# Optimization experiments

Hardware: AMD Instinct MI355X
Metric: run time of the kernel (lower is better)

Reference implementation:

```python
import jax, jax.numpy as jnp
import numpy as np

H = 128          # hidden_channels
K = 3            # TAGConv hops
NV, NS = 100000, 50000
EVV, ESS, EH, EIN = 1_000_000, 500_000, 500_000, 300_000


def setup_inputs() -> dict:
    key = jax.random.key(0)
    ks = iter(jax.random.split(key, 40))
    def rn(shape, s=0.05):
        return jax.random.normal(next(ks), shape, jnp.float32) * s
    def ri(shape, hi):
        return jax.random.randint(next(ks), shape, 0, hi, jnp.int32)
    return {
        "game_x": rn((NV, 5), 1.0),
        "state_x": rn((NS, 6), 1.0),
        "edge_index_v_v": ri((2, EVV), NV),
        "edge_type_v_v": ri((EVV,), 4),  # unused in forward (interface fidelity)
        "edge_index_history_v_s": jnp.stack([ri((EH,), NV), ri((EH,), NS)]),
        "edge_attr_history_v_s": rn((EH, 1), 1.0),
        "edge_index_in_v_s": jnp.stack([ri((EIN,), NV), ri((EIN,), NS)]),
        "edge_index_s_s": ri((2, ESS), NS),
        # TAGConv weights: (K+1) hop linears, shared bias
        "tag1_W": rn((K + 1, 5, H)), "tag1_b": rn((H,)),
        "tag2_W": rn((K + 1, 6, H)), "tag2_b": rn((H,)),
        # 7 SAGEConv layers stacked: gv[1:3]=0,1; sv[1:3]=2,3; in1=4; sv2=5,6
        "sage_Wl": rn((7, H, H)), "sage_bl": rn((7, H)), "sage_Wr": rn((7, H, H)),
        # GATConv (1 head, edge_dim=1)
        "gat_Wsrc": rn((H, H)), "gat_Wdst": rn((H, H)), "gat_We": rn((1, H)),
        "gat_asrc": rn((H,)), "gat_adst": rn((H,)), "gat_ae": rn((H,)), "gat_b": rn((H,)),
        # final MLP: single Linear(H, 1)
        "mlp_W": rn((H, 1)), "mlp_b": rn((1,)),
    }


def _seg_sum(x, idx, n):
    return jax.ops.segment_sum(x, idx, num_segments=n)


def tag_conv(x, edge_index, n, W, b):
    """TAGConv: out = sum_k lin_k(A_norm^k x) + b, gcn_norm w/o self loops."""
    src, dst = edge_index[0], edge_index[1]
    deg = _seg_sum(jnp.ones(src.shape, x.dtype), dst, n)
    dinv = jnp.where(deg > 0, jax.lax.rsqrt(jnp.maximum(deg, 1.0)), 0.0)
    norm = dinv[src] * dinv[dst]                      # [E]
    out = x @ W[0]
    h = x
    for k in range(1, W.shape[0]):
        h = _seg_sum(h[src] * norm[:, None], dst, n)  # one hop of normalized A
        out = out + h @ W[k]
    return out + b


def sage_conv(x_src, x_dst, edge_index, n_dst, Wl, bl, Wr):
    """SAGEConv(mean): lin_l(mean_j x_src[j]) + lin_r(x_dst)."""
    src, dst = edge_index[0], edge_index[1]
    s = _seg_sum(x_src[src], dst, n_dst)
    cnt = _seg_sum(jnp.ones(src.shape, x_src.dtype), dst, n_dst)
    mean = s / jnp.maximum(cnt, 1.0)[:, None]
    return mean @ Wl + bl + x_dst @ Wr


def gat_conv(x_src, x_dst, edge_index, edge_attr, n_dst,
             Wsrc, Wdst, We, asrc, adst, ae, b):
    """Bipartite GATConv, 1 head, edge features, no self loops."""
    src, dst = edge_index[0], edge_index[1]
    hs = x_src @ Wsrc                                  # [NV, H]
    hd = x_dst @ Wdst                                  # [NS, H]
    a = (hs @ asrc)[src] + (hd @ adst)[dst] + (edge_attr @ We) @ ae  # [E]
    a = jax.nn.leaky_relu(a, 0.2)
    m = jax.ops.segment_max(a, dst, num_segments=n_dst)
    e = jnp.exp(a - m[dst])                            # segment softmax
    denom = _seg_sum(e, dst, n_dst)
    alpha = e / jnp.maximum(denom, 1e-16)[dst]
    out = _seg_sum(alpha[:, None] * hs[src], dst, n_dst)
    return out + b


def reference(game_x, state_x, edge_index_v_v, edge_type_v_v,
              edge_index_history_v_s, edge_attr_history_v_s,
              edge_index_in_v_s, edge_index_s_s,
              tag1_W, tag1_b, tag2_W, tag2_b,
              sage_Wl, sage_bl, sage_Wr,
              gat_Wsrc, gat_Wdst, gat_We, gat_asrc, gat_adst, gat_ae, gat_b,
              mlp_W, mlp_b):
    relu = jax.nn.relu
    nv, ns = game_x.shape[0], state_x.shape[0]
    # game-vertex tower
    gx = relu(tag_conv(game_x, edge_index_v_v, nv, tag1_W, tag1_b))
    for i in range(2):
        gx = relu(sage_conv(gx, gx, edge_index_v_v, nv, sage_Wl[i], sage_bl[i], sage_Wr[i]))
    # state-vertex tower
    sx = relu(tag_conv(state_x, edge_index_s_s, ns, tag2_W, tag2_b))
    for i in range(2, 4):
        sx = relu(sage_conv(sx, sx, edge_index_s_s, ns, sage_Wl[i], sage_bl[i], sage_Wr[i]))
    # bipartite attention game -> state
    hist = relu(gat_conv(gx, sx, edge_index_history_v_s, edge_attr_history_v_s, ns,
                         gat_Wsrc, gat_Wdst, gat_We, gat_asrc, gat_adst, gat_ae, gat_b))
    in_x = relu(sage_conv(gx, hist, edge_index_in_v_s, ns, sage_Wl[4], sage_bl[4], sage_Wr[4]))
    # second state tower
    sx = in_x
    for i in range(5, 7):
        sx = relu(sage_conv(sx, sx, edge_index_s_s, ns, sage_Wl[i], sage_bl[i], sage_Wr[i]))
    return sx @ mlp_W + mlp_b                          # [NS, 1]
```

## Files before the change

kernel.cpp:

```cpp
#include <hip/hip_runtime.h>

#define H 128
typedef unsigned short u16;
typedef __attribute__((ext_vector_type(8))) short bf16x8;
typedef __attribute__((ext_vector_type(4))) float f32x4;


static inline int gridFor(long long work, int block, int cap = 8192){
  long long g = (work + block - 1) / block;
  if (g > cap) g = cap;
  if (g < 1) g = 1;
  return (int)g;
}

__device__ __forceinline__ float waveReduceSum(float v){
  #pragma unroll
  for(int off = 32; off > 0; off >>= 1) v += __shfl_down(v, off);
  return v;
}

__device__ __forceinline__ float bflo(unsigned v){ return __uint_as_float(v << 16); }
__device__ __forceinline__ float bfhi(unsigned v){ return __uint_as_float(v & 0xffff0000u); }
__device__ __forceinline__ u16 f2bf(float f){
  unsigned u = __float_as_uint(f);
  return (u16)((u + 0x7fffu + ((u >> 16) & 1u)) >> 16);
}
__device__ __forceinline__ unsigned pack2(float lo, float hi){
  return (unsigned)f2bf(lo) | ((unsigned)f2bf(hi) << 16);
}

#define BSHIFT 9
#define CH 2048

template<bool HAS_ATTR>
__global__ __launch_bounds__(256) void part_kernel(
    const int* __restrict__ src, const int* __restrict__ dst,
    const float* __restrict__ attr, int* __restrict__ bcur,
    int2* __restrict__ bpairs, float* __restrict__ battr, int E, int cap){
  __shared__ int hist[256];
  __shared__ int hscan[256];
  __shared__ int hbase[256];
  __shared__ int hcur[256];
  __shared__ int2 buf[CH];
  __shared__ float abuf[HAS_ATTR ? CH : 1];

  const int t = threadIdx.x;
  const int e0 = blockIdx.x * CH;
  const int cnt = min(CH, E - e0);

  hist[t] = 0; hcur[t] = 0;
  __syncthreads();

  #pragma unroll
  for(int j = 0; j < 8; j++){
    int i = e0 + j*256 + t;
    if(i - e0 < cnt) atomicAdd(&hist[dst[i] >> BSHIFT], 1);
  }
  __syncthreads();

  {
    int v = hist[t];
    int lane = t & 63, wid = t >> 6;
    int incl = v;
    #pragma unroll
    for(int off = 1; off < 64; off <<= 1){
      int u = __shfl_up(incl, off);
      if(lane >= off) incl += u;
    }
    __shared__ int ws4[4];
    if(lane == 63) ws4[wid] = incl;
    __syncthreads();
    int wofs = 0;
    for(int wj = 0; wj < wid; wj++) wofs += ws4[wj];
    hscan[t] = wofs + incl - v;
    hbase[t] = (v > 0) ? atomicAdd(&bcur[t], v) : 0;
  }
  __syncthreads();

  #pragma unroll
  for(int j = 0; j < 8; j++){
    int i = e0 + j*256 + t;
    if(i - e0 < cnt){
      int d = dst[i], s = src[i];
      int b = d >> BSHIFT;
      int lp = atomicAdd(&hcur[b], 1);
      int slot = hscan[b] + lp;
      buf[slot] = make_int2(d, s);
      if(HAS_ATTR) abuf[slot] = attr[i];
    }
  }
  __syncthreads();

  for(int u = t; u < cnt; u += 256){
    int2 pr = buf[u];
    int b = pr.x >> BSHIFT;
    int g = b * cap + hbase[b] + (u - hscan[b]);
    bpairs[g] = pr;
    if(HAS_ATTR) battr[g] = abuf[u];
  }
}

__global__ void bucket_scan(const int* __restrict__ bcur, int* __restrict__ bbase,
                            int* __restrict__ rp0, int* __restrict__ rp1,
                            int* __restrict__ rp2, int* __restrict__ rp3,
                            int n0, int n1, int n2, int n3){
  int g = blockIdx.x;
  int n = (g == 0) ? n0 : (g == 1) ? n1 : (g == 2) ? n2 : n3;
  int* rowp = (g == 0) ? rp0 : (g == 1) ? rp1 : (g == 2) ? rp2 : rp3;
  int NB = (n + 511) >> BSHIFT;
  int t = threadIdx.x;
  int v = (t < NB) ? bcur[g*256 + t] : 0;
  int lane = t & 63, wid = t >> 6;
  int incl = v;
  #pragma unroll
  for(int off = 1; off < 64; off <<= 1){
    int u = __shfl_up(incl, off);
    if(lane >= off) incl += u;
  }
  __shared__ int ws4[4];
  if(lane == 63) ws4[wid] = incl;
  __syncthreads();
  int wofs = 0;
  for(int wj = 0; wj < wid; wj++) wofs += ws4[wj];
  bbase[g*256 + t] = wofs + incl - v;
  if(t == 0) rowp[n] = ws4[0] + ws4[1] + ws4[2] + ws4[3];
}

template<bool HAS_ATTR, bool DINV>
__global__ __launch_bounds__(256) void build_kernel(
    const int2* __restrict__ bpairs, const float* __restrict__ battr,
    const int* __restrict__ bcur, const int* __restrict__ bbase,
    int* __restrict__ rowp, int* __restrict__ col, float* __restrict__ attrp,
    float* __restrict__ dinv, int cap, int n){
  __shared__ int hist[512];
  __shared__ int hcur[512];
  __shared__ int ws4[4];

  const int b = blockIdx.x;
  const int t = threadIdx.x;
  const int d0 = b << BSHIFT;
  const int dn = min(512, n - d0);
  const int cnt = bcur[b];
  const int base = bbase[b];
  const int2* ep = bpairs + (size_t)b * cap;

  hist[t] = 0; hist[t + 256] = 0;
  __syncthreads();
  for(int u = t; u < cnt; u += 256) atomicAdd(&hist[ep[u].x - d0], 1);
  __syncthreads();

  int a0 = hist[2*t], a1 = hist[2*t + 1];
  int s = a0 + a1;
  int lane = t & 63, wid = t >> 6;
  int incl = s;
  #pragma unroll
  for(int off = 1; off < 64; off <<= 1){
    int u = __shfl_up(incl, off);
    if(lane >= off) incl += u;
  }
  if(lane == 63) ws4[wid] = incl;
  __syncthreads();
  int wofs = 0;
  for(int wj = 0; wj < wid; wj++) wofs += ws4[wj];
  int excl = wofs + incl - s;
  __syncthreads();
  hcur[2*t] = excl; hcur[2*t + 1] = excl + a0;
  if(2*t < dn){
    rowp[d0 + 2*t] = base + excl;
    if(DINV) dinv[d0 + 2*t] = a0 > 0 ? rsqrtf((float)a0) : 0.f;
  }
  if(2*t + 1 < dn){
    rowp[d0 + 2*t + 1] = base + excl + a0;
    if(DINV) dinv[d0 + 2*t + 1] = a1 > 0 ? rsqrtf((float)a1) : 0.f;
  }
  __syncthreads();

  for(int u = t; u < cnt; u += 256){
    int2 pr = ep[u];
    int pos = base + atomicAdd(&hcur[pr.x - d0], 1);
    col[pos] = pr.y;
    if(HAS_ATTR) attrp[pos] = battr[(size_t)b * cap + u];
  }
}


__global__ void cvt_weights(const float* __restrict__ Wl, const float* __restrict__ Wr,
                            const float* __restrict__ Wsrc, u16* __restrict__ Wb){
  const int total = 15 * H * H;
  for(int t = blockIdx.x*blockDim.x + threadIdx.x; t < total; t += gridDim.x*blockDim.x){
    int mat = t >> 14, idx = t & 16383;
    int k = idx >> 7, colj = idx & 127;
    const float* srcp = (mat < 7) ? (Wl + ((size_t)mat << 14))
                       : (mat < 14) ? (Wr + ((size_t)(mat - 7) << 14))
                       : Wsrc;
    Wb[((size_t)mat << 14) + (size_t)colj*H + k] = f2bf(srcp[idx]);
  }
}

__global__ void mat_vec_row(const float* __restrict__ W, const float* __restrict__ a,
                            float* __restrict__ outv){
  int k = threadIdx.x;
  if(k < H){
    float s = 0.f;
    for(int j = 0; j < H; j++) s += W[(size_t)k*H + j] * a[j];
    outv[k] = s;
  }
}

__global__ void dot128(const float* __restrict__ a, const float* __restrict__ b,
                       float* __restrict__ o){
  int l = threadIdx.x;
  float acc = a[l]*b[l] + a[l+64]*b[l+64];
  acc = waveReduceSum(acc);
  if(l == 0) o[0] = acc;
}


template<int C>
__global__ void csr_tag_hop(const int* __restrict__ rowp, const int* __restrict__ col,
                            const float* __restrict__ dinv,
                            const float* __restrict__ hin, int sin,
                            float* __restrict__ hout, int N){
  for(int i = blockIdx.x*blockDim.x + threadIdx.x; i < N; i += gridDim.x*blockDim.x){
    int b = rowp[i], e = rowp[i+1];
    float dd = dinv[i];
    float acc0[C], acc1[C];
    #pragma unroll
    for(int k = 0; k < C; k++){ acc0[k] = 0.f; acc1[k] = 0.f; }
    int p = b;
    for(; p + 2 <= e; p += 2){
      int s0 = col[p], s1 = col[p+1];
      float n0 = dinv[s0] * dd, n1 = dinv[s1] * dd;
      #pragma unroll
      for(int k = 0; k < C; k++){
        acc0[k] += hin[(size_t)s0*sin + k] * n0;
        acc1[k] += hin[(size_t)s1*sin + k] * n1;
      }
    }
    if(p < e){
      int s0 = col[p];
      float n0 = dinv[s0] * dd;
      #pragma unroll
      for(int k = 0; k < C; k++) acc0[k] += hin[(size_t)s0*sin + k] * n0;
    }
    #pragma unroll
    for(int k = 0; k < C; k++) hout[(size_t)i*8 + k] = acc0[k] + acc1[k];
  }
}

template<int C>
__global__ __launch_bounds__(256) void tag_fuse(
    const float* __restrict__ x, const float* __restrict__ h1,
    const float* __restrict__ h2, const float* __restrict__ h3,
    const float* __restrict__ W, const float* __restrict__ bias,
    u16* __restrict__ out, int N){
  __shared__ float Ws[4*C*H];
  for(int u = threadIdx.x; u < 4*C*H; u += 256) Ws[u] = W[u];
  __syncthreads();
  const long long total = (long long)N * H;
  for(long long t = (long long)blockIdx.x*blockDim.x + threadIdx.x; t < total;
      t += (long long)gridDim.x*blockDim.x){
    int i = (int)(t >> 7), j = (int)(t & 127);
    const float* xr = x + (size_t)i*C;
    const float* r1 = h1 + (size_t)i*8;
    const float* r2 = h2 + (size_t)i*8;
    const float* r3 = h3 + (size_t)i*8;
    float acc = bias[j];
    #pragma unroll
    for(int k = 0; k < C; k++) acc += xr[k] * Ws[k*H + j];
    #pragma unroll
    for(int k = 0; k < C; k++) acc += r1[k] * Ws[(C + k)*H + j];
    #pragma unroll
    for(int k = 0; k < C; k++) acc += r2[k] * Ws[(2*C + k)*H + j];
    #pragma unroll
    for(int k = 0; k < C; k++) acc += r3[k] * Ws[(3*C + k)*H + j];
    out[t] = f2bf(fmaxf(acc, 0.f));
  }
}


__global__ __launch_bounds__(256) void sage_fused(
    const u16* __restrict__ G, const u16* __restrict__ X,
    const int* __restrict__ rowp, const int* __restrict__ col,
    const u16* __restrict__ WbR, const u16* __restrict__ WbL,
    const float* __restrict__ bl, u16* __restrict__ out, int N){
  __shared__ u16 Ws[H * H];

  const int t = threadIdx.x;
  const int lane = t & 63;
  const int wib = t >> 6;
  const int m0 = (blockIdx.x * 4 + wib) * 32;
  const int r16 = lane & 15;
  const int kg  = (lane >> 4) * 8;
  const bool active = (m0 < N);

  for(int u = t; u < H*H/8; u += 256){
    bf16x8 v = *(const bf16x8*)&WbR[u*8];
    int c = u >> 4, kb = (u & 15) * 16;
    *(bf16x8*)((char*)Ws + c*256 + (kb ^ ((c & 7) << 4))) = v;
  }
  __syncthreads();

  f32x4 acc[2][8];
  #pragma unroll
  for(int rt = 0; rt < 2; rt++)
    #pragma unroll
    for(int tt = 0; tt < 8; tt++) acc[rt][tt] = (f32x4){0.f,0.f,0.f,0.f};

  if(active){
    #pragma unroll
    for(int k0c = 0; k0c < 4; k0c++){
      int k0 = k0c * 32;
      bf16x8 af[2];
      #pragma unroll
      for(int rt = 0; rt < 2; rt++){
        int row = m0 + rt*16 + r16;
        if(row < N) af[rt] = *(const bf16x8*)&X[(size_t)row*H + k0 + kg];
        else        af[rt] = (bf16x8){0,0,0,0,0,0,0,0};
      }
      #pragma unroll
      for(int tt = 0; tt < 8; tt++){
        int c = tt*16 + r16;
        int kb = (k0 + kg)*2;
        bf16x8 bf = *(const bf16x8*)((char*)Ws + c*256 + (kb ^ ((c & 7) << 4)));
        acc[0][tt] = __builtin_amdgcn_mfma_f32_16x16x32_bf16(af[0], bf, acc[0][tt], 0, 0, 0);
        acc[1][tt] = __builtin_amdgcn_mfma_f32_16x16x32_bf16(af[1], bf, acc[1][tt], 0, 0, 0);
      }
    }
  }
  __syncthreads();

  for(int u = t; u < H*H/8; u += 256){
    bf16x8 v = *(const bf16x8*)&WbL[u*8];
    int c = u >> 4, kb = (u & 15) * 16;
    *(bf16x8*)((char*)Ws + c*256 + (kb ^ ((c & 7) << 4))) = v;
  }
  __syncthreads();

  if(active){
    #pragma unroll
    for(int rt = 0; rt < 2; rt++){
      int row = m0 + rt*16 + r16;
      float ag[4][8];
      #pragma unroll
      for(int kc = 0; kc < 4; kc++)
        #pragma unroll
        for(int j = 0; j < 8; j++) ag[kc][j] = 0.f;

      if(row < N){
        int b = rowp[row], e = rowp[row+1];
        for(int p = b; p < e; p++){
          int s = col[p];
          const u16* gr = &G[(size_t)s*H + kg];
          #pragma unroll
          for(int kc = 0; kc < 4; kc++){
            bf16x8 v = *(const bf16x8*)(gr + kc*32);
            const unsigned* vu = (const unsigned*)&v;
            #pragma unroll
            for(int q = 0; q < 4; q++){
              ag[kc][2*q]   += bflo(vu[q]);
              ag[kc][2*q+1] += bfhi(vu[q]);
            }
          }
        }
        float inv = 1.f / fmaxf((float)(e - b), 1.f);
        #pragma unroll
        for(int kc = 0; kc < 4; kc++)
          #pragma unroll
          for(int j = 0; j < 8; j++) ag[kc][j] *= inv;
      }

      #pragma unroll
      for(int kc = 0; kc < 4; kc++){
        unsigned uu[4];
        #pragma unroll
        for(int q = 0; q < 4; q++) uu[q] = pack2(ag[kc][2*q], ag[kc][2*q+1]);
        bf16x8 agb = *(bf16x8*)uu;
        int kb = (kc*32 + kg)*2;
        #pragma unroll
        for(int tt = 0; tt < 8; tt++){
          int c = tt*16 + r16;
          bf16x8 bf = *(const bf16x8*)((char*)Ws + c*256 + (kb ^ ((c & 7) << 4)));
          acc[rt][tt] = __builtin_amdgcn_mfma_f32_16x16x32_bf16(agb, bf, acc[rt][tt], 0, 0, 0);
        }
      }
    }

    #pragma unroll
    for(int rt = 0; rt < 2; rt++){
      const int orow = m0 + rt*16 + (lane >> 4) * 4;
      #pragma unroll
      for(int tt = 0; tt < 8; tt++){
        int c = tt*16 + r16;
        float bb = bl[c];
        #pragma unroll
        for(int r = 0; r < 4; r++){
          if(orow + r < N){
            float v = fmaxf(acc[rt][tt][r] + bb, 0.f);
            out[(size_t)(orow + r)*H + c] = f2bf(v);
          }
        }
      }
    }
  }
}


__global__ __launch_bounds__(256) void gemm_mfma(
    const u16* __restrict__ x, const u16* __restrict__ Wb,
    u16* __restrict__ out, int N){
  __shared__ u16 Ws[H * H];
  const int t = threadIdx.x;
  for(int u = t; u < H*H/8; u += 256){
    bf16x8 v = *(const bf16x8*)&Wb[u*8];
    int c = u >> 4, kb = (u & 15) * 16;
    *(bf16x8*)((char*)Ws + c*256 + (kb ^ ((c & 7) << 4))) = v;
  }
  __syncthreads();

  const int lane = t & 63;
  const int wib = t >> 6;
  const int m0 = (blockIdx.x * 4 + wib) * 32;
  if(m0 >= N) return;
  const int r16 = lane & 15;
  const int kg = (lane >> 4) * 8;

  f32x4 acc[2][8];
  #pragma unroll
  for(int rt = 0; rt < 2; rt++)
    #pragma unroll
    for(int tt = 0; tt < 8; tt++) acc[rt][tt] = (f32x4){0.f,0.f,0.f,0.f};

  #pragma unroll
  for(int k0c = 0; k0c < 4; k0c++){
    int k0 = k0c * 32;
    bf16x8 af[2];
    #pragma unroll
    for(int rt = 0; rt < 2; rt++){
      int row = m0 + rt*16 + r16;
      if(row < N) af[rt] = *(const bf16x8*)&x[(size_t)row*H + k0 + kg];
      else        af[rt] = (bf16x8){0,0,0,0,0,0,0,0};
    }
    #pragma unroll
    for(int tt = 0; tt < 8; tt++){
      int c = tt*16 + r16;
      int kb = (k0 + kg)*2;
      bf16x8 bf = *(const bf16x8*)((char*)Ws + c*256 + (kb ^ ((c & 7) << 4)));
      acc[0][tt] = __builtin_amdgcn_mfma_f32_16x16x32_bf16(af[0], bf, acc[0][tt], 0, 0, 0);
      acc[1][tt] = __builtin_amdgcn_mfma_f32_16x16x32_bf16(af[1], bf, acc[1][tt], 0, 0, 0);
    }
  }

  #pragma unroll
  for(int rt = 0; rt < 2; rt++){
    const int orow = m0 + rt*16 + (lane >> 4) * 4;
    #pragma unroll
    for(int tt = 0; tt < 8; tt++){
      int c = tt*16 + r16;
      #pragma unroll
      for(int r = 0; r < 4; r++){
        if(orow + r < N)
          out[(size_t)(orow + r)*H + c] = f2bf(acc[rt][tt][r]);
      }
    }
  }
}


__global__ void rowdot_bf(const u16* __restrict__ x, const float* __restrict__ v,
                          float* __restrict__ out, int N){
  int lane = threadIdx.x & 63;
  int w = (blockIdx.x*blockDim.x + threadIdx.x) >> 6;
  int nw = (gridDim.x*blockDim.x) >> 6;
  for(int i = w; i < N; i += nw){
    unsigned u = *(const unsigned*)&x[(size_t)i*H + lane*2];
    float acc = bflo(u)*v[lane*2] + bfhi(u)*v[lane*2 + 1];
    acc = waveReduceSum(acc);
    if(lane == 0) out[i] = acc;
  }
}

__global__ void gat_fused(const int* __restrict__ rowp, const int* __restrict__ colv,
                          const float* __restrict__ attrp, const float* __restrict__ av,
                          const float* __restrict__ ad, const float* __restrict__ cptr,
                          const u16* __restrict__ hs, const float* __restrict__ bias,
                          u16* __restrict__ out, int N){
  const float c = cptr[0];
  int lane = threadIdx.x & 63;
  int w = (blockIdx.x*blockDim.x + threadIdx.x) >> 6;
  int nw = (gridDim.x*blockDim.x) >> 6;
  for(int i = w; i < N; i += nw){
    int b = rowp[i], e = rowp[i+1];
    float adi = ad[i];
    float accx0 = 0.f, accy0 = 0.f, accx1 = 0.f, accy1 = 0.f;
    float sume = 0.f;
    int p = b;
    for(; p + 2 <= e; p += 2){
      int s0 = colv[p], s1 = colv[p+1];
      float a0 = av[s0] + adi + attrp[p] * c;
      float a1 = av[s1] + adi + attrp[p+1] * c;
      a0 = a0 > 0.f ? a0 : 0.2f * a0;
      a1 = a1 > 0.f ? a1 : 0.2f * a1;
      float e0 = __expf(a0), e1 = __expf(a1);
      unsigned v0 = *(const unsigned*)&hs[(size_t)s0*H + lane*2];
      unsigned v1 = *(const unsigned*)&hs[(size_t)s1*H + lane*2];
      accx0 += e0 * bflo(v0); accy0 += e0 * bfhi(v0);
      accx1 += e1 * bflo(v1); accy1 += e1 * bfhi(v1);
      sume += e0 + e1;
    }
    if(p < e){
      int s0 = colv[p];
      float a0 = av[s0] + adi + attrp[p] * c;
      a0 = a0 > 0.f ? a0 : 0.2f * a0;
      float e0 = __expf(a0);
      unsigned v0 = *(const unsigned*)&hs[(size_t)s0*H + lane*2];
      accx0 += e0 * bflo(v0); accy0 += e0 * bfhi(v0);
      sume += e0;
    }
    float rd = 1.f / fmaxf(sume, 1e-16f);
    float ox = fmaxf((accx0 + accx1) * rd + bias[lane*2],     0.f);
    float oy = fmaxf((accy0 + accy1) * rd + bias[lane*2 + 1], 0.f);
    *(unsigned*)&out[(size_t)i*H + lane*2] = pack2(ox, oy);
  }
}

__global__ void mlp_out_bf(const u16* __restrict__ x, const float* __restrict__ W,
                           const float* __restrict__ b, float* __restrict__ out, int N){
  int lane = threadIdx.x & 63;
  int w = (blockIdx.x*blockDim.x + threadIdx.x) >> 6;
  int nw = (gridDim.x*blockDim.x) >> 6;
  for(int i = w; i < N; i += nw){
    unsigned u = *(const unsigned*)&x[(size_t)i*H + lane*2];
    float acc = bflo(u)*W[lane*2] + bfhi(u)*W[lane*2 + 1];
    acc = waveReduceSum(acc);
    if(lane == 0) out[i] = acc + b[0];
  }
}


extern "C" void kernel_launch(void* const* d_in, const int* in_sizes, int n_in,
                              void* d_out, int out_size, void* d_ws, size_t ws_size,
                              hipStream_t stream) {
  const float* game_x  = (const float*)d_in[0];
  const float* state_x = (const float*)d_in[1];
  const int*   e_vv    = (const int*)d_in[2];
  const int*   e_hist  = (const int*)d_in[4];
  const float* attr_h  = (const float*)d_in[5];
  const int*   e_in    = (const int*)d_in[6];
  const int*   e_ss    = (const int*)d_in[7];
  const float* tag1_W  = (const float*)d_in[8];
  const float* tag1_b  = (const float*)d_in[9];
  const float* tag2_W  = (const float*)d_in[10];
  const float* tag2_b  = (const float*)d_in[11];
  const float* sage_Wl = (const float*)d_in[12];
  const float* sage_bl = (const float*)d_in[13];
  const float* sage_Wr = (const float*)d_in[14];
  const float* gat_Wsrc= (const float*)d_in[15];
  const float* gat_Wdst= (const float*)d_in[16];
  const float* gat_We  = (const float*)d_in[17];
  const float* gat_asrc= (const float*)d_in[18];
  const float* gat_adst= (const float*)d_in[19];
  const float* gat_ae  = (const float*)d_in[20];
  const float* gat_b   = (const float*)d_in[21];
  const float* mlp_W   = (const float*)d_in[22];
  const float* mlp_b   = (const float*)d_in[23];
  float* out = (float*)d_out;

  const int NV  = in_sizes[0] / 5;
  const int NS  = in_sizes[1] / 6;
  const int EVV = in_sizes[2] / 2;
  const int EH  = in_sizes[4] / 2;
  const int EIN = in_sizes[6] / 2;
  const int ESS = in_sizes[7] / 2;

  const int* vv_src = e_vv;   const int* vv_dst = e_vv + EVV;
  const int* eh_src = e_hist; const int* eh_dst = e_hist + EH;
  const int* in_src = e_in;   const int* in_dst = e_in + EIN;
  const int* ss_src = e_ss;   const int* ss_dst = e_ss + ESS;

  const int NBv = (NV + 511) >> BSHIFT;
  const int NBs = (NS + 511) >> BSHIFT;
  const int capvv = (EVV / NBv) * 3 / 2 + 64;
  const int capss = (ESS / NBs) * 3 / 2 + 64;
  const int capeh = (EH  / NBs) * 3 / 2 + 64;
  const int capin = (EIN / NBs) * 3 / 2 + 64;

  char* wp = (char*)d_ws;
  auto alloc = [&](size_t bytes) -> void* {
    void* p = (void*)wp;
    wp += (bytes + 511) & ~size_t(511);
    return p;
  };
  u16* V0 = (u16*)alloc((size_t)NV*H*2);
  u16* V1 = (u16*)alloc((size_t)NV*H*2);
  u16* S0 = (u16*)alloc((size_t)NS*H*2);
  u16* S1 = (u16*)alloc((size_t)NS*H*2);
  u16* Wb = (u16*)alloc((size_t)15*H*H*2);
  float* dinv_v = (float*)alloc((size_t)NV*4);
  float* dinv_s = (float*)alloc((size_t)NS*4);
  float* av   = (float*)alloc((size_t)NV*4);
  float* ad   = (float*)alloc((size_t)NS*4);
  float* h5a  = (float*)alloc((size_t)NV*8*4);
  float* h5b  = (float*)alloc((size_t)NV*8*4);
  float* h5c  = (float*)alloc((size_t)NV*8*4);
  float* h6a  = (float*)alloc((size_t)NS*8*4);
  float* h6b  = (float*)alloc((size_t)NS*8*4);
  float* h6c  = (float*)alloc((size_t)NS*8*4);
  float* wvec = (float*)alloc(H*4);
  float* cbuf = (float*)alloc(4);
  int* vv_rowp = (int*)alloc((size_t)(NV+1)*4);
  int* vv_col  = (int*)alloc((size_t)EVV*4);
  int* ss_rowp = (int*)alloc((size_t)(NS+1)*4);
  int* ss_col  = (int*)alloc((size_t)ESS*4);
  int* eh_rowp = (int*)alloc((size_t)(NS+1)*4);
  int* eh_col  = (int*)alloc((size_t)EH*4);
  float* eh_attr = (float*)alloc((size_t)EH*4);
  int* in_rowp = (int*)alloc((size_t)(NS+1)*4);
  int* in_col  = (int*)alloc((size_t)EIN*4);
  int2* vv_bp = (int2*)alloc((size_t)NBv*capvv*8);
  int2* ss_bp = (int2*)alloc((size_t)NBs*capss*8);
  int2* eh_bp = (int2*)alloc((size_t)NBs*capeh*8);
  int2* in_bp = (int2*)alloc((size_t)NBs*capin*8);
  float* eh_ba = (float*)alloc((size_t)NBs*capeh*4);
  int* bcur  = (int*)alloc(4*256*4);
  int* bbase = (int*)alloc(4*256*4);
  (void)ws_size; (void)n_in; (void)out_size;

  const int B = 256;
  #define GRID1(n) gridFor((long long)(n), B), B, 0, stream
  #define GRIDW(e) gridFor((long long)(e) * 64, B, 8192), B, 0, stream
  #define GEMM(n)  ((n) + 127) / 128, 256, 0, stream

  hipMemsetAsync(bcur, 0, 4*256*4, stream);
  part_kernel<false><<<(EVV + CH - 1)/CH, 256, 0, stream>>>(
      vv_src, vv_dst, nullptr, bcur + 0,   vv_bp, nullptr, EVV, capvv);
  part_kernel<false><<<(ESS + CH - 1)/CH, 256, 0, stream>>>(
      ss_src, ss_dst, nullptr, bcur + 256, ss_bp, nullptr, ESS, capss);
  part_kernel<true ><<<(EH  + CH - 1)/CH, 256, 0, stream>>>(
      eh_src, eh_dst, attr_h,  bcur + 512, eh_bp, eh_ba,   EH,  capeh);
  part_kernel<false><<<(EIN + CH - 1)/CH, 256, 0, stream>>>(
      in_src, in_dst, nullptr, bcur + 768, in_bp, nullptr, EIN, capin);
  bucket_scan<<<4, 256, 0, stream>>>(bcur, bbase, vv_rowp, ss_rowp, eh_rowp, in_rowp,
                                     NV, NS, NS, NS);
  build_kernel<false,true ><<<NBv, 256, 0, stream>>>(
      vv_bp, nullptr, bcur + 0,   bbase + 0,   vv_rowp, vv_col, nullptr, dinv_v, capvv, NV);
  build_kernel<false,true ><<<NBs, 256, 0, stream>>>(
      ss_bp, nullptr, bcur + 256, bbase + 256, ss_rowp, ss_col, nullptr, dinv_s, capss, NS);
  build_kernel<true ,false><<<NBs, 256, 0, stream>>>(
      eh_bp, eh_ba,   bcur + 512, bbase + 512, eh_rowp, eh_col, eh_attr, nullptr, capeh, NS);
  build_kernel<false,false><<<NBs, 256, 0, stream>>>(
      in_bp, nullptr, bcur + 768, bbase + 768, in_rowp, in_col, nullptr, nullptr, capin, NS);

  cvt_weights<<<GRID1(15*H*H)>>>(sage_Wl, sage_Wr, gat_Wsrc, Wb);
  mat_vec_row<<<1, 128, 0, stream>>>(gat_Wdst, gat_adst, wvec);
  dot128<<<1, 64, 0, stream>>>(gat_We, gat_ae, cbuf);

  #define WBL(l) (Wb + ((size_t)(l) << 14))
  #define WBR(l) (Wb + ((size_t)(7 + (l)) << 14))

  csr_tag_hop<5><<<GRID1(NV)>>>(vv_rowp, vv_col, dinv_v, game_x, 5, h5a, NV);
  csr_tag_hop<5><<<GRID1(NV)>>>(vv_rowp, vv_col, dinv_v, h5a, 8, h5b, NV);
  csr_tag_hop<5><<<GRID1(NV)>>>(vv_rowp, vv_col, dinv_v, h5b, 8, h5c, NV);
  tag_fuse<5><<<GRID1((long long)NV*H)>>>(game_x, h5a, h5b, h5c, tag1_W, tag1_b, V0, NV);

  sage_fused<<<GEMM(NV)>>>(V0, V0, vv_rowp, vv_col, WBR(0), WBL(0),
                           sage_bl + 0*H, V1, NV);
  sage_fused<<<GEMM(NV)>>>(V1, V1, vv_rowp, vv_col, WBR(1), WBL(1),
                           sage_bl + 1*H, V0, NV);

  csr_tag_hop<6><<<GRID1(NS)>>>(ss_rowp, ss_col, dinv_s, state_x, 6, h6a, NS);
  csr_tag_hop<6><<<GRID1(NS)>>>(ss_rowp, ss_col, dinv_s, h6a, 8, h6b, NS);
  csr_tag_hop<6><<<GRID1(NS)>>>(ss_rowp, ss_col, dinv_s, h6b, 8, h6c, NS);
  tag_fuse<6><<<GRID1((long long)NS*H)>>>(state_x, h6a, h6b, h6c, tag2_W, tag2_b, S0, NS);

  sage_fused<<<GEMM(NS)>>>(S0, S0, ss_rowp, ss_col, WBR(2), WBL(2),
                           sage_bl + 2*H, S1, NS);
  sage_fused<<<GEMM(NS)>>>(S1, S1, ss_rowp, ss_col, WBR(3), WBL(3),
                           sage_bl + 3*H, S0, NS);

  gemm_mfma<<<GEMM(NV)>>>(V0, Wb + ((size_t)14 << 14), V1, NV);
  rowdot_bf<<<GRIDW(NV)>>>(V1, gat_asrc, av, NV);
  rowdot_bf<<<GRIDW(NS)>>>(S0, wvec, ad, NS);
  gat_fused<<<GRIDW(NS)>>>(eh_rowp, eh_col, eh_attr, av, ad, cbuf, V1, gat_b, S1, NS);

  sage_fused<<<GEMM(NS)>>>(V0, S1, in_rowp, in_col, WBR(4), WBL(4),
                           sage_bl + 4*H, S0, NS);

  sage_fused<<<GEMM(NS)>>>(S0, S0, ss_rowp, ss_col, WBR(5), WBL(5),
                           sage_bl + 5*H, S1, NS);
  sage_fused<<<GEMM(NS)>>>(S1, S1, ss_rowp, ss_col, WBR(6), WBL(6),
                           sage_bl + 6*H, S0, NS);

  mlp_out_bf<<<GRIDW(NS)>>>(S0, mlp_W, mlp_b, out, NS);

  #undef GRID1
  #undef GRIDW
  #undef GEMM
  #undef WBL
  #undef WBR
}
```

Before: 898.2 us.

## Halve rows per wave in sage_fused and pack dinv into TAG hop rows

sage_fused now processes 16 rows per wave instead of 32 and launches twice as many blocks. The intent is more parallelism for the latency-bound neighbour gather, at the cost of loading the 32KB weight tile into shared memory twice as often. The TAG hops now store dinv in slot 7 of each 8-float row, so one gathered row supplies both features and normaliser and the separate dinv gather goes away. A pack pass is added to lay out the input that way. The cap on grid-stride warp kernels is also raised.

```diff
diff --git a/kernel.cpp b/kernel.cpp
--- a/kernel.cpp
+++ b/kernel.cpp
@@ -6,7 +6,7 @@
 typedef __attribute__((ext_vector_type(4))) float f32x4;
 
 
-static inline int gridFor(long long work, int block, int cap = 8192){
+static inline int gridFor(long long work, int block, int cap = 16384){
   long long g = (work + block - 1) / block;
   if (g > cap) g = cap;
   if (g < 1) g = 1;
@@ -217,34 +217,44 @@
 
 
 template<int C>
-__global__ void csr_tag_hop(const int* __restrict__ rowp, const int* __restrict__ col,
-                            const float* __restrict__ dinv,
-                            const float* __restrict__ hin, int sin,
-                            float* __restrict__ hout, int N){
+__global__ void pack_rows(const float* __restrict__ x, const float* __restrict__ dinv,
+                          float* __restrict__ xp, int N){
+  for(int i = blockIdx.x*blockDim.x + threadIdx.x; i < N; i += gridDim.x*blockDim.x){
+    #pragma unroll
+    for(int k = 0; k < C; k++) xp[(size_t)i*8 + k] = x[(size_t)i*C + k];
+    xp[(size_t)i*8 + 7] = dinv[i];
+  }
+}
+
+template<int C>
+__global__ void csr_tag_hop8(const int* __restrict__ rowp, const int* __restrict__ col,
+                             const float* __restrict__ hin, float* __restrict__ hout, int N){
   for(int i = blockIdx.x*blockDim.x + threadIdx.x; i < N; i += gridDim.x*blockDim.x){
     int b = rowp[i], e = rowp[i+1];
-    float dd = dinv[i];
+    float dd = hin[(size_t)i*8 + 7];
     float acc0[C], acc1[C];
     #pragma unroll
     for(int k = 0; k < C; k++){ acc0[k] = 0.f; acc1[k] = 0.f; }
     int p = b;
     for(; p + 2 <= e; p += 2){
-      int s0 = col[p], s1 = col[p+1];
-      float n0 = dinv[s0] * dd, n1 = dinv[s1] * dd;
+      const float* r0 = &hin[(size_t)col[p]   * 8];
+      const float* r1 = &hin[(size_t)col[p+1] * 8];
+      float w0 = r0[7] * dd, w1 = r1[7] * dd;
       #pragma unroll
       for(int k = 0; k < C; k++){
-        acc0[k] += hin[(size_t)s0*sin + k] * n0;
-        acc1[k] += hin[(size_t)s1*sin + k] * n1;
+        acc0[k] += r0[k] * w0;
+        acc1[k] += r1[k] * w1;
       }
     }
     if(p < e){
-      int s0 = col[p];
-      float n0 = dinv[s0] * dd;
-      #pragma unroll
-      for(int k = 0; k < C; k++) acc0[k] += hin[(size_t)s0*sin + k] * n0;
+      const float* r0 = &hin[(size_t)col[p] * 8];
+      float w0 = r0[7] * dd;
+      #pragma unroll
+      for(int k = 0; k < C; k++) acc0[k] += r0[k] * w0;
     }
     #pragma unroll
     for(int k = 0; k < C; k++) hout[(size_t)i*8 + k] = acc0[k] + acc1[k];
+    hout[(size_t)i*8 + 7] = dd;
   }
 }
 
@@ -289,10 +299,11 @@
   const int t = threadIdx.x;
   const int lane = t & 63;
   const int wib = t >> 6;
-  const int m0 = (blockIdx.x * 4 + wib) * 32;
+  const int m0 = (blockIdx.x * 4 + wib) * 16;
   const int r16 = lane & 15;
   const int kg  = (lane >> 4) * 8;
   const bool active = (m0 < N);
+  const int row = m0 + r16;
 
   for(int u = t; u < H*H/8; u += 256){
     bf16x8 v = *(const bf16x8*)&WbR[u*8];
@@ -301,30 +312,23 @@
   }
   __syncthreads();
 
-  f32x4 acc[2][8];
-  #pragma unroll
-  for(int rt = 0; rt < 2; rt++)
-    #pragma unroll
-    for(int tt = 0; tt < 8; tt++) acc[rt][tt] = (f32x4){0.f,0.f,0.f,0.f};
+  f32x4 acc[8];
+  #pragma unroll
+  for(int tt = 0; tt < 8; tt++) acc[tt] = (f32x4){0.f,0.f,0.f,0.f};
 
   if(active){
     #pragma unroll
     for(int k0c = 0; k0c < 4; k0c++){
       int k0 = k0c * 32;
-      bf16x8 af[2];
-      #pragma unroll
-      for(int rt = 0; rt < 2; rt++){
-        int row = m0 + rt*16 + r16;
-        if(row < N) af[rt] = *(const bf16x8*)&X[(size_t)row*H + k0 + kg];
-        else        af[rt] = (bf16x8){0,0,0,0,0,0,0,0};
-      }
+      bf16x8 af;
+      if(row < N) af = *(const bf16x8*)&X[(size_t)row*H + k0 + kg];
+      else        af = (bf16x8){0,0,0,0,0,0,0,0};
       #pragma unroll
       for(int tt = 0; tt < 8; tt++){
         int c = tt*16 + r16;
         int kb = (k0 + kg)*2;
         bf16x8 bf = *(const bf16x8*)((char*)Ws + c*256 + (kb ^ ((c & 7) << 4)));
-        acc[0][tt] = __builtin_amdgcn_mfma_f32_16x16x32_bf16(af[0], bf, acc[0][tt], 0, 0, 0);
-        acc[1][tt] = __builtin_amdgcn_mfma_f32_16x16x32_bf16(af[1], bf, acc[1][tt], 0, 0, 0);
+        acc[tt] = __builtin_amdgcn_mfma_f32_16x16x32_bf16(af, bf, acc[tt], 0, 0, 0);
       }
     }
   }
@@ -338,67 +342,60 @@
   __syncthreads();
 
   if(active){
-    #pragma unroll
-    for(int rt = 0; rt < 2; rt++){
-      int row = m0 + rt*16 + r16;
-      float ag[4][8];
+    float ag[4][8];
+    #pragma unroll
+    for(int kc = 0; kc < 4; kc++)
+      #pragma unroll
+      for(int j = 0; j < 8; j++) ag[kc][j] = 0.f;
+
+    if(row < N){
+      int b = rowp[row], e = rowp[row+1];
+      for(int p = b; p < e; p++){
+        int s = col[p];
+        const u16* gr = &G[(size_t)s*H + kg];
+        #pragma unroll
+        for(int kc = 0; kc < 4; kc++){
+          bf16x8 v = *(const bf16x8*)(gr + kc*32);
+          const unsigned* vu = (const unsigned*)&v;
+          #pragma unroll
+          for(int q = 0; q < 4; q++){
+            ag[kc][2*q]   += bflo(vu[q]);
+            ag[kc][2*q+1] += bfhi(vu[q]);
+          }
+        }
+      }
+      float inv = 1.f / fmaxf((float)(e - b), 1.f);
       #pragma unroll
       for(int kc = 0; kc < 4; kc++)
         #pragma unroll
-        for(int j = 0; j < 8; j++) ag[kc][j] = 0.f;
-
-      if(row < N){
-        int b = rowp[row], e = rowp[row+1];
-        for(int p = b; p < e; p++){
-          int s = col[p];
-          const u16* gr = &G[(size_t)s*H + kg];
-          #pragma unroll
-          for(int kc = 0; kc < 4; kc++){
-            bf16x8 v = *(const bf16x8*)(gr + kc*32);
-            const unsigned* vu = (const unsigned*)&v;
-            #pragma unroll
-            for(int q = 0; q < 4; q++){
-              ag[kc][2*q]   += bflo(vu[q]);
-              ag[kc][2*q+1] += bfhi(vu[q]);
-            }
-          }
-        }
-        float inv = 1.f / fmaxf((float)(e - b), 1.f);
-        #pragma unroll
-        for(int kc = 0; kc < 4; kc++)
-          #pragma unroll
-          for(int j = 0; j < 8; j++) ag[kc][j] *= inv;
-      }
-
-      #pragma unroll
-      for(int kc = 0; kc < 4; kc++){
-        unsigned uu[4];
-        #pragma unroll
-        for(int q = 0; q < 4; q++) uu[q] = pack2(ag[kc][2*q], ag[kc][2*q+1]);
-        bf16x8 agb = *(bf16x8*)uu;
-        int kb = (kc*32 + kg)*2;
-        #pragma unroll
-        for(int tt = 0; tt < 8; tt++){
-          int c = tt*16 + r16;
-          bf16x8 bf = *(const bf16x8*)((char*)Ws + c*256 + (kb ^ ((c & 7) << 4)));
-          acc[rt][tt] = __builtin_amdgcn_mfma_f32_16x16x32_bf16(agb, bf, acc[rt][tt], 0, 0, 0);
-        }
-      }
-    }
-
-    #pragma unroll
-    for(int rt = 0; rt < 2; rt++){
-      const int orow = m0 + rt*16 + (lane >> 4) * 4;
+        for(int j = 0; j < 8; j++) ag[kc][j] *= inv;
+    }
+
+    #pragma unroll
+    for(int kc = 0; kc < 4; kc++){
+      unsigned uu[4];
+      #pragma unroll
+      for(int q = 0; q < 4; q++) uu[q] = pack2(ag[kc][2*q], ag[kc][2*q+1]);
+      bf16x8 agb = *(bf16x8*)uu;
+      int kb = (kc*32 + kg)*2;
       #pragma unroll
       for(int tt = 0; tt < 8; tt++){
         int c = tt*16 + r16;
-        float bb = bl[c];
-        #pragma unroll
-        for(int r = 0; r < 4; r++){
-          if(orow + r < N){
-            float v = fmaxf(acc[rt][tt][r] + bb, 0.f);
-            out[(size_t)(orow + r)*H + c] = f2bf(v);
-          }
+        bf16x8 bf = *(const bf16x8*)((char*)Ws + c*256 + (kb ^ ((c & 7) << 4)));
+        acc[tt] = __builtin_amdgcn_mfma_f32_16x16x32_bf16(agb, bf, acc[tt], 0, 0, 0);
+      }
+    }
+
+    const int orow = m0 + (lane >> 4) * 4;
+    #pragma unroll
+    for(int tt = 0; tt < 8; tt++){
+      int c = tt*16 + r16;
+      float bb = bl[c];
+      #pragma unroll
+      for(int r = 0; r < 4; r++){
+        if(orow + r < N){
+          float v = fmaxf(acc[tt][r] + bb, 0.f);
+          out[(size_t)(orow + r)*H + c] = f2bf(v);
         }
       }
     }
@@ -600,9 +597,11 @@
   float* dinv_s = (float*)alloc((size_t)NS*4);
   float* av   = (float*)alloc((size_t)NV*4);
   float* ad   = (float*)alloc((size_t)NS*4);
+  float* xp5  = (float*)alloc((size_t)NV*8*4);
   float* h5a  = (float*)alloc((size_t)NV*8*4);
   float* h5b  = (float*)alloc((size_t)NV*8*4);
   float* h5c  = (float*)alloc((size_t)NV*8*4);
+  float* xp6  = (float*)alloc((size_t)NS*8*4);
   float* h6a  = (float*)alloc((size_t)NS*8*4);
   float* h6b  = (float*)alloc((size_t)NS*8*4);
   float* h6c  = (float*)alloc((size_t)NS*8*4);
@@ -627,9 +626,9 @@
   (void)ws_size; (void)n_in; (void)out_size;
 
   const int B = 256;
-  #define GRID1(n) gridFor((long long)(n), B), B, 0, stream
-  #define GRIDW(e) gridFor((long long)(e) * 64, B, 8192), B, 0, stream
-  #define GEMM(n)  ((n) + 127) / 128, 256, 0, stream
+  #define GRID1(n) gridFor((long long)(n), B, 8192), B, 0, stream
+  #define GRIDW(e) gridFor((long long)(e) * 64, B, 16384), B, 0, stream
+  #define GEMM(n)  ((n) + 63) / 64, 256, 0, stream
 
   hipMemsetAsync(bcur, 0, 4*256*4, stream);
   part_kernel<false><<<(EVV + CH - 1)/CH, 256, 0, stream>>>(
@@ -658,9 +657,10 @@
   #define WBL(l) (Wb + ((size_t)(l) << 14))
   #define WBR(l) (Wb + ((size_t)(7 + (l)) << 14))
 
-  csr_tag_hop<5><<<GRID1(NV)>>>(vv_rowp, vv_col, dinv_v, game_x, 5, h5a, NV);
-  csr_tag_hop<5><<<GRID1(NV)>>>(vv_rowp, vv_col, dinv_v, h5a, 8, h5b, NV);
-  csr_tag_hop<5><<<GRID1(NV)>>>(vv_rowp, vv_col, dinv_v, h5b, 8, h5c, NV);
+  pack_rows<5><<<GRID1(NV)>>>(game_x, dinv_v, xp5, NV);
+  csr_tag_hop8<5><<<GRID1(NV)>>>(vv_rowp, vv_col, xp5, h5a, NV);
+  csr_tag_hop8<5><<<GRID1(NV)>>>(vv_rowp, vv_col, h5a, h5b, NV);
+  csr_tag_hop8<5><<<GRID1(NV)>>>(vv_rowp, vv_col, h5b, h5c, NV);
   tag_fuse<5><<<GRID1((long long)NV*H)>>>(game_x, h5a, h5b, h5c, tag1_W, tag1_b, V0, NV);
 
   sage_fused<<<GEMM(NV)>>>(V0, V0, vv_rowp, vv_col, WBR(0), WBL(0),
@@ -668,9 +668,10 @@
   sage_fused<<<GEMM(NV)>>>(V1, V1, vv_rowp, vv_col, WBR(1), WBL(1),
                            sage_bl + 1*H, V0, NV);
 
-  csr_tag_hop<6><<<GRID1(NS)>>>(ss_rowp, ss_col, dinv_s, state_x, 6, h6a, NS);
-  csr_tag_hop<6><<<GRID1(NS)>>>(ss_rowp, ss_col, dinv_s, h6a, 8, h6b, NS);
-  csr_tag_hop<6><<<GRID1(NS)>>>(ss_rowp, ss_col, dinv_s, h6b, 8, h6c, NS);
+  pack_rows<6><<<GRID1(NS)>>>(state_x, dinv_s, xp6, NS);
+  csr_tag_hop8<6><<<GRID1(NS)>>>(ss_rowp, ss_col, xp6, h6a, NS);
+  csr_tag_hop8<6><<<GRID1(NS)>>>(ss_rowp, ss_col, h6a, h6b, NS);
+  csr_tag_hop8<6><<<GRID1(NS)>>>(ss_rowp, ss_col, h6b, h6c, NS);
   tag_fuse<6><<<GRID1((long long)NS*H)>>>(state_x, h6a, h6b, h6c, tag2_W, tag2_b, S0, NS);
 
   sage_fused<<<GEMM(NS)>>>(S0, S0, ss_rowp, ss_col, WBR(2), WBL(2),
@@ -678,7 +679,7 @@
   sage_fused<<<GEMM(NS)>>>(S1, S1, ss_rowp, ss_col, WBR(3), WBL(3),
                            sage_bl + 3*H, S0, NS);
 
-  gemm_mfma<<<GEMM(NV)>>>(V0, Wb + ((size_t)14 << 14), V1, NV);
+  gemm_mfma<<<((NV + 127)/128), 256, 0, stream>>>(V0, Wb + ((size_t)14 << 14), V1, NV);
   rowdot_bf<<<GRIDW(NV)>>>(V1, gat_asrc, av, NV);
   rowdot_bf<<<GRIDW(NS)>>>(S0, wvec, ad, NS);
   gat_fused<<<GRIDW(NS)>>>(eh_rowp, eh_col, eh_attr, av, ad, cbuf, V1, gat_b, S1, NS);
```

New measurement: 908.8 us. No clear change (+1.2%).
